# Kernel tuning notes

Hardware: AMD Instinct MI355X
Metric: run time of the kernel (lower is better)

Reference implementation:

```python
import jax, jax.numpy as jnp
import numpy as np
import math

DIM = 768
HEADS = 12
HEAD_DIM = DIM // HEADS
LENS_T = 64
LENS_S = 256
NTOK = LENS_T + LENS_S
BATCH = 32
MLP_HIDDEN = 4 * DIM
KEEP_RATIO = 0.7
LENS_KEEP = math.ceil(KEEP_RATIO * LENS_S)  # 180, static
NEG_INF = -1e9  # finite stand-in for masked_fill(-inf); mask is all-False here
LN_EPS = 1e-5


def layer_norm(x, g, b):
    m = jnp.mean(x, axis=-1, keepdims=True)
    v = jnp.var(x, axis=-1, keepdims=True)
    return (x - m) * jax.lax.rsqrt(v + LN_EPS) * g + b


def attention(x_normed, w_qkv, w_proj, b_proj, mask):
    # x_normed: [B,N,C]; torch: qkv Linear (no bias), split heads, softmax(qk*scale), proj
    B, N, C = x_normed.shape
    qkv = (x_normed @ w_qkv.T).reshape(B, N, 3, HEADS, HEAD_DIM)
    qkv = jnp.transpose(qkv, (2, 0, 3, 1, 4))  # [3,B,H,N,Dh]
    q, k, v = qkv[0], qkv[1], qkv[2]
    scores = jnp.einsum('bhqd,bhkd->bhqk', q, k) * (HEAD_DIM ** -0.5)
    scores = jnp.where(mask[:, None, None, :], NEG_INF, scores)
    attn = jax.nn.softmax(scores, axis=-1)  # [B,H,N,N]
    out = jnp.einsum('bhqk,bhkd->bhqd', attn, v)
    out = jnp.transpose(out, (0, 2, 1, 3)).reshape(B, N, C)
    return out @ w_proj.T + b_proj, attn


def mlp(x, w_fc1, b_fc1, w_fc2, b_fc2):
    h = jax.nn.gelu(x @ w_fc1.T + b_fc1, approximate=False)
    return h @ w_fc2.T + b_fc2


def candidate_topk(attn_all, tmpl_mask_f):
    # attn_all: [B,H,N,N]; template->search block, masked mean over template rows,
    # mean over heads, sort descending, split into keep/removed.
    attn_ts = attn_all[:, :, :LENS_T, LENS_T:]  # [B,H,T,S]
    w = tmpl_mask_f[:, None, :, None]  # [B,1,T,1]
    denom = jnp.sum(tmpl_mask_f, axis=1)[:, None, None]  # [B,1,1]
    scores = jnp.sum(attn_ts * w, axis=2) / denom  # [B,H,S] mean over kept template rows
    scores = jnp.mean(scores, axis=1)  # [B,S] mean over heads
    order = jnp.argsort(-scores, axis=1)  # descending
    return order[:, :LENS_KEEP], order[:, LENS_KEEP:]


def gather_tokens(tokens, topk_idx):
    tokens_t = tokens[:, :LENS_T]
    tokens_s = tokens[:, LENS_T:]
    kept = jnp.take_along_axis(tokens_s, topk_idx[:, :, None], axis=1)
    return jnp.concatenate([tokens_t, kept], axis=1)


def setup_inputs() -> dict:
    key = jax.random.key(0)
    ks = jax.random.split(key, 12)
    s = 0.02
    return {
        'x_rgb': jax.random.normal(ks[0], (BATCH, NTOK, DIM), jnp.float32),
        'x_tir': jax.random.normal(ks[1], (BATCH, NTOK, DIM), jnp.float32),
        'global_index_t': jax.random.randint(ks[2], (BATCH, LENS_T), 0, 64).astype(jnp.int64),
        'global_index_s': jax.random.randint(ks[3], (BATCH, LENS_S), 0, 256).astype(jnp.int64),
        'mask': jnp.zeros((BATCH, NTOK), dtype=bool),
        'cte_template_mask': jnp.ones((BATCH, LENS_T), dtype=bool),
        'keep_ratio_search': 0,
        'js_loss': jax.random.normal(ks[4], (1,), jnp.float32),
        'g1': jnp.ones((DIM,), jnp.float32),
        'b1': jnp.zeros((DIM,), jnp.float32),
        'w_qkv': jax.random.normal(ks[5], (3 * DIM, DIM), jnp.float32) * s,
        'w_proj': jax.random.normal(ks[6], (DIM, DIM), jnp.float32) * s,
        'b_proj': jnp.zeros((DIM,), jnp.float32),
        'g2': jnp.ones((DIM,), jnp.float32),
        'b2': jnp.zeros((DIM,), jnp.float32),
        'w_fc1': jax.random.normal(ks[7], (MLP_HIDDEN, DIM), jnp.float32) * s,
        'b_fc1': jnp.zeros((MLP_HIDDEN,), jnp.float32),
        'w_fc2': jax.random.normal(ks[8], (DIM, MLP_HIDDEN), jnp.float32) * s,
        'b_fc2': jnp.zeros((DIM,), jnp.float32),
    }


def reference(x_rgb, x_tir, global_index_t, global_index_s, mask, cte_template_mask,
              keep_ratio_search, js_loss, g1, b1, w_qkv, w_proj, b_proj, g2, b2,
              w_fc1, b_fc1, w_fc2, b_fc2):
    # dual-stream shared-weight attention
    rgb_attn_out, corrmap_rgb = attention(layer_norm(x_rgb, g1, b1), w_qkv, w_proj, b_proj, mask)
    tir_attn_out, corrmap_tir = attention(layer_norm(x_tir, g1, b1), w_qkv, w_proj, b_proj, mask)
    x_rgb = x_rgb + rgb_attn_out  # drop_path = Identity
    x_tir = x_tir + tir_attn_out

    # candidate elimination: both streams use the SAME fused attention map,
    # so the topk is identical for rgb and tir (torch calls it twice, same result)
    attn_all = corrmap_rgb + corrmap_tir
    tmpl_mask_f = cte_template_mask.astype(attn_all.dtype)
    topk_idx, non_topk_idx = candidate_topk(attn_all, tmpl_mask_f)
    x_rgb = gather_tokens(x_rgb, topk_idx)
    x_tir = gather_tokens(x_tir, topk_idx)
    global_index_s_new = jnp.take_along_axis(global_index_s, topk_idx, axis=1)
    removed_index_s = jnp.take_along_axis(global_index_s, non_topk_idx, axis=1)

    x_rgb = x_rgb + mlp(layer_norm(x_rgb, g2, b2), w_fc1, b_fc1, w_fc2, b_fc2)
    x_tir = x_tir + mlp(layer_norm(x_tir, g2, b2), w_fc1, b_fc1, w_fc2, b_fc2)
    return (x_rgb, x_tir, global_index_t, global_index_s_new, removed_index_s,
            corrmap_rgb, corrmap_tir, js_loss)
```

## Files before the change

### kernel.cpp

```cpp
#include <hip/hip_runtime.h>

typedef long long LL;
typedef unsigned short ushort_t;
typedef __attribute__((ext_vector_type(8))) short bfrag;
typedef __attribute__((ext_vector_type(8))) _Float16 hfrag;
typedef __attribute__((ext_vector_type(4))) float facc;
typedef __attribute__((ext_vector_type(4))) unsigned short us4;

constexpr int CDIM  = 768;
constexpr int HEADS = 12;
constexpr int LT    = 64;
constexpr int NTOK  = 320;
constexpr int BATCH = 32;
constexpr int LKEEP = 180;
constexpr int LREM  = 76;
constexpr int NK    = 244;

constexpr LL O_XRGB = 0;
constexpr LL O_XTIR = 5996544;
constexpr LL O_GIT  = 11993088;
constexpr LL O_GSN  = 11995136;
constexpr LL O_REM  = 12000896;
constexpr LL O_CR   = 12003328;
constexpr LL O_CT   = 51324928;
constexpr LL O_JS   = 90646528;

constexpr LL W_X1   = 0;
constexpr LL W_X1G  = 15728640;
constexpr LL W_XN   = 27746304;
constexpr LL W_QKV  = 35610624;
constexpr LL W_ATT  = 59596800;

constexpr LL SZH = 7864320;

__device__ inline ushort_t cvt_bf16(float f) {
    union { float f; unsigned u; } x; x.f = f;
    unsigned u = x.u + 0x7fffu + ((x.u >> 16) & 1u);
    return (ushort_t)(u >> 16);
}
union h16u { _Float16 h; ushort_t u; };

#define GLL(gp, lp) __builtin_amdgcn_global_load_lds( \
    (const __attribute__((address_space(1))) unsigned int*)(gp), \
    (__attribute__((address_space(3))) unsigned int*)(lp), 16, 0, 0)

template<bool B16OUT>
__global__ __launch_bounds__(256)
void ln_kernel(const float* __restrict__ x, const float* __restrict__ g,
               const float* __restrict__ bta, void* __restrict__ y)
{
    LL row = blockIdx.x;
    const float* xr = x + row * 768;
    int t = threadIdx.x;
    float v0 = xr[t], v1 = xr[t + 256], v2 = xr[t + 512];
    __shared__ float red[256];
    red[t] = v0 + v1 + v2;
    __syncthreads();
    for (int s = 128; s; s >>= 1) { if (t < s) red[t] += red[t + s]; __syncthreads(); }
    float mean = red[0] / 768.0f;
    __syncthreads();
    float d0 = v0 - mean, d1 = v1 - mean, d2 = v2 - mean;
    red[t] = d0 * d0 + d1 * d1 + d2 * d2;
    __syncthreads();
    for (int s = 128; s; s >>= 1) { if (t < s) red[t] += red[t + s]; __syncthreads(); }
    float var = red[0] / 768.0f;
    float rs = 1.0f / sqrtf(var + 1e-5f);
    float o0 = d0 * rs * g[t]       + bta[t];
    float o1 = d1 * rs * g[t + 256] + bta[t + 256];
    float o2 = d2 * rs * g[t + 512] + bta[t + 512];
    if (B16OUT) {
        ushort_t* yr = (ushort_t*)y + row * 768;
        yr[t] = cvt_bf16(o0); yr[t + 256] = cvt_bf16(o1); yr[t + 512] = cvt_bf16(o2);
    } else {
        float* yr = (float*)y + row * 768;
        yr[t] = o0; yr[t + 256] = o1; yr[t + 512] = o2;
    }
}

__global__ __launch_bounds__(256)
void ln_f16x2(const float* __restrict__ x, const float* __restrict__ g,
              const float* __restrict__ bta,
              ushort_t* __restrict__ yh, ushort_t* __restrict__ yl)
{
    LL row = blockIdx.x;
    const float* xr = x + row * 768;
    int t = threadIdx.x;
    float v0 = xr[t], v1 = xr[t + 256], v2 = xr[t + 512];
    __shared__ float red[256];
    red[t] = v0 + v1 + v2;
    __syncthreads();
    for (int s = 128; s; s >>= 1) { if (t < s) red[t] += red[t + s]; __syncthreads(); }
    float mean = red[0] / 768.0f;
    __syncthreads();
    float d0 = v0 - mean, d1 = v1 - mean, d2 = v2 - mean;
    red[t] = d0 * d0 + d1 * d1 + d2 * d2;
    __syncthreads();
    for (int s = 128; s; s >>= 1) { if (t < s) red[t] += red[t + s]; __syncthreads(); }
    float var = red[0] / 768.0f;
    float rs = 1.0f / sqrtf(var + 1e-5f);
    #pragma unroll
    for (int c = 0; c < 3; ++c) {
        float d = (c == 0 ? d0 : c == 1 ? d1 : d2);
        int idx = t + c * 256;
        float o = d * rs * g[idx] + bta[idx];
        h16u hi, lo;
        hi.h = (_Float16)o;
        lo.h = (_Float16)(o - (float)hi.h);
        yh[row * 768 + idx] = hi.u;
        yl[row * 768 + idx] = lo.u;
    }
}

__global__ __launch_bounds__(256)
void cvt_f16x2(const float* __restrict__ in, ushort_t* __restrict__ oh,
               ushort_t* __restrict__ ol, int n)
{
    int i = (blockIdx.x * 256 + threadIdx.x) * 4;
    if (i >= n) return;
    float4 v = *(const float4*)(in + i);
    us4 h, l;
    #pragma unroll
    for (int j = 0; j < 4; ++j) {
        float f = (j == 0 ? v.x : j == 1 ? v.y : j == 2 ? v.z : v.w);
        h16u hh, ll;
        hh.h = (_Float16)f;
        ll.h = (_Float16)(f - (float)hh.h);
        h[j] = hh.u; l[j] = ll.u;
    }
    *(us4*)(oh + i) = h;
    *(us4*)(ol + i) = l;
}

__global__ __launch_bounds__(256)
void gemm_qkv(const ushort_t* __restrict__ Ah, const ushort_t* __restrict__ Al,
              const ushort_t* __restrict__ Bh, const ushort_t* __restrict__ Bl,
              ushort_t* __restrict__ Q1, ushort_t* __restrict__ Q2,
              ushort_t* __restrict__ K1, ushort_t* __restrict__ K2,
              ushort_t* __restrict__ Vt)
{
    __shared__ ushort_t Ahs[8192], Als[8192], Bhs[8192], Bls[8192];
    const int t = threadIdx.x;
    const int wave = t >> 6, lane = t & 63;
    const int wr = wave >> 1, wc = wave & 1;
    const int lr = lane & 15, lh = lane >> 4;
    const LL bm = (LL)blockIdx.y * 128, bn = (LL)blockIdx.x * 128;
    const bool vt = (blockIdx.x >= 12);

    facc acc[4][4];
    #pragma unroll
    for (int i = 0; i < 4; ++i)
        #pragma unroll
        for (int j = 0; j < 4; ++j) acc[i][j] = (facc)(0.0f);

    const LL soff = (bm + wave * 16 + (lane >> 2)) * (LL)768 + (lane & 3) * 8;
    const LL boff = (bn + wave * 16 + (lane >> 2)) * (LL)768 + (lane & 3) * 8;
    const LL a64 = (LL)64 * 768;

    GLL(Ah + soff,       &Ahs[wave * 512]);
    GLL(Ah + soff + a64, &Ahs[2048 + wave * 512]);
    GLL(Bh + boff,       &Bhs[wave * 512]);
    GLL(Bh + boff + a64, &Bhs[2048 + wave * 512]);
    if (!vt) {
        GLL(Al + soff,       &Als[wave * 512]);
        GLL(Al + soff + a64, &Als[2048 + wave * 512]);
        GLL(Bl + boff,       &Bls[wave * 512]);
        GLL(Bl + boff + a64, &Bls[2048 + wave * 512]);
    }
    __syncthreads();

    int cur = 0;
    for (int k0 = 0; k0 < 768; k0 += 32) {
        int nb = (cur ^ 1) * 4096;
        if (k0 + 32 < 768) {
            GLL(Ah + soff + k0 + 32,       &Ahs[nb + wave * 512]);
            GLL(Ah + soff + k0 + 32 + a64, &Ahs[nb + 2048 + wave * 512]);
            GLL(Bh + boff + k0 + 32,       &Bhs[nb + wave * 512]);
            GLL(Bh + boff + k0 + 32 + a64, &Bhs[nb + 2048 + wave * 512]);
            if (!vt) {
                GLL(Al + soff + k0 + 32,       &Als[nb + wave * 512]);
                GLL(Al + soff + k0 + 32 + a64, &Als[nb + 2048 + wave * 512]);
                GLL(Bl + boff + k0 + 32,       &Bls[nb + wave * 512]);
                GLL(Bl + boff + k0 + 32 + a64, &Bls[nb + 2048 + wave * 512]);
            }
        }
        int cb = cur * 4096;
        hfrag ah[4], bh[4];
        #pragma unroll
        for (int mi = 0; mi < 4; ++mi)
            ah[mi] = *(const hfrag*)&Ahs[cb + (wr * 64 + mi * 16 + lr) * 32 + lh * 8];
        #pragma unroll
        for (int ni = 0; ni < 4; ++ni)
            bh[ni] = *(const hfrag*)&Bhs[cb + (wc * 64 + ni * 16 + lr) * 32 + lh * 8];
        if (!vt) {
            hfrag al[4], bl[4];
            #pragma unroll
            for (int mi = 0; mi < 4; ++mi)
                al[mi] = *(const hfrag*)&Als[cb + (wr * 64 + mi * 16 + lr) * 32 + lh * 8];
            #pragma unroll
            for (int ni = 0; ni < 4; ++ni)
                bl[ni] = *(const hfrag*)&Bls[cb + (wc * 64 + ni * 16 + lr) * 32 + lh * 8];
            #pragma unroll
            for (int mi = 0; mi < 4; ++mi)
                #pragma unroll
                for (int ni = 0; ni < 4; ++ni) {
                    acc[mi][ni] = __builtin_amdgcn_mfma_f32_16x16x32_f16(al[mi], bh[ni], acc[mi][ni], 0, 0, 0);
                    acc[mi][ni] = __builtin_amdgcn_mfma_f32_16x16x32_f16(ah[mi], bl[ni], acc[mi][ni], 0, 0, 0);
                    acc[mi][ni] = __builtin_amdgcn_mfma_f32_16x16x32_f16(ah[mi], bh[ni], acc[mi][ni], 0, 0, 0);
                }
        } else {
            #pragma unroll
            for (int mi = 0; mi < 4; ++mi)
                #pragma unroll
                for (int ni = 0; ni < 4; ++ni)
                    acc[mi][ni] = __builtin_amdgcn_mfma_f32_16x16x32_f16(ah[mi], bh[ni], acc[mi][ni], 0, 0, 0);
        }
        __syncthreads();
        cur ^= 1;
    }

    #pragma unroll
    for (int mi = 0; mi < 4; ++mi)
        #pragma unroll
        for (int ni = 0; ni < 4; ++ni)
            #pragma unroll
            for (int j = 0; j < 4; ++j) {
                int r = (int)bm + wr * 64 + mi * 16 + lh * 4 + j;
                int c = (int)bn + wc * 64 + ni * 16 + lr;
                int b = r / 320, tt = r - b * 320;
                int s = c / 768, rem = c - s * 768;
                int h = rem >> 6, d = rem & 63;
                LL hb = (LL)(b * 12 + h) * 20480;
                float v = acc[mi][ni][j];
                if (s == 2) {
                    Vt[hb + d * 320 + tt] = cvt_bf16(v);
                } else {
                    h16u a1, a2;
                    a1.h = (_Float16)v;
                    a2.h = (_Float16)(v - (float)a1.h);
                    LL idx = hb + (LL)tt * 64 + d;
                    if (s == 0) { Q1[idx] = a1.u; Q2[idx] = a2.u; }
                    else        { K1[idx] = a1.u; K2[idx] = a2.u; }
                }
            }
}

__global__ __launch_bounds__(256, 2)
void fused_attn(const ushort_t* __restrict__ Qh, const ushort_t* __restrict__ Qm,
                const ushort_t* __restrict__ Kh, const ushort_t* __restrict__ Km,
                const ushort_t* __restrict__ Vt,
                float* __restrict__ corr, ushort_t* __restrict__ attb,
                double* __restrict__ part, int mod)
{
    __shared__ __align__(128) unsigned char lds[81920];
    constexpr int PS = 40960;

    const int t = threadIdx.x;
    const int wave = t >> 6, lane = t & 63;
    const int lr = lane & 15, lh = lane >> 4;
    const int id  = blockIdx.x;
    const int xcd = id & 7;
    const int rem = id >> 3;
    const int grp = rem / 5;
    const int r0i = rem - grp * 5;
    const int bh  = grp * 8 + xcd;
    const int b = bh / 12, h = bh - b * 12;
    const int r0 = r0i * 64;
    const LL kvbase = (LL)bh * 20480;

    const LL qoff = kvbase + (LL)(r0 + wave * 16 + lr) * 64 + lh * 8;
    hfrag qh0 = *(const hfrag*)(Qh + qoff), qh1 = *(const hfrag*)(Qh + qoff + 32);
    hfrag qm0 = *(const hfrag*)(Qm + qoff), qm1 = *(const hfrag*)(Qm + qoff + 32);

    facc sacc[20];
    #pragma unroll
    for (int ct = 0; ct < 20; ++ct) sacc[ct] = (facc)(0.0f);

    #pragma unroll
    for (int ha = 0; ha < 5; ++ha) {
        if (ha) __syncthreads();
        #pragma unroll
        for (int i = 0; i < 4; ++i) {
            int id2 = wave * 4 + i;
            int s = id2 >> 3, c = id2 & 7;
            int local = c * 1024 + lane * 16;
            int row = local >> 7;
            int sb = local ^ ((row & 7) << 4);
            LL src = kvbase + (LL)ha * 4096 + (sb >> 1);
            const ushort_t* kp = (s == 0) ? Kh : Km;
            GLL(kp + src, &lds[s * 8192 + c * 1024]);
        }
        __syncthreads();

        #pragma unroll
        for (int ctl = 0; ctl < 4; ++ctl) {
            int tokl = ctl * 16 + lr;
            int x = (tokl & 7) << 4;
            const unsigned char* kb = lds + tokl * 128;
            int o0 = (lh * 16) ^ x;
            int o1 = (64 + lh * 16) ^ x;
            hfrag kh0 = *(const hfrag*)(kb + o0);
            hfrag kh1 = *(const hfrag*)(kb + o1);
            hfrag km0 = *(const hfrag*)(kb + 8192 + o0);
            hfrag km1 = *(const hfrag*)(kb + 8192 + o1);
            facc a = sacc[ha * 4 + ctl];
            a = __builtin_amdgcn_mfma_f32_16x16x32_f16(qm0, kh0, a, 0, 0, 0);
            a = __builtin_amdgcn_mfma_f32_16x16x32_f16(qh0, km0, a, 0, 0, 0);
            a = __builtin_amdgcn_mfma_f32_16x16x32_f16(qh0, kh0, a, 0, 0, 0);
            a = __builtin_amdgcn_mfma_f32_16x16x32_f16(qm1, kh1, a, 0, 0, 0);
            a = __builtin_amdgcn_mfma_f32_16x16x32_f16(qh1, km1, a, 0, 0, 0);
            a = __builtin_amdgcn_mfma_f32_16x16x32_f16(qh1, kh1, a, 0, 0, 0);
            sacc[ha * 4 + ctl] = a;
        }
    }

    __syncthreads();

    #pragma unroll
    for (int i = 0; i < 10; ++i) {
        int chunk = wave * 10 + i;
        int gs = chunk * 1024 + lane * 16;
        int d = gs / 640;
        int w = gs - d * 640;
        int sb = d * 640 + (w ^ ((d & 7) << 4));
        GLL(Vt + kvbase + (sb >> 1), &lds[chunk * 1024]);
    }

    float rs4[4];
    #pragma unroll
    for (int j = 0; j < 4; ++j) {
        float m = sacc[0][j];
        #pragma unroll
        for (int ct = 1; ct < 20; ++ct) m = fmaxf(m, sacc[ct][j]);
        #pragma unroll
        for (int o = 1; o < 16; o <<= 1) m = fmaxf(m, __shfl_xor(m, o, 64));
        m *= 0.125f;
        float s = 0.0f;
        #pragma unroll
        for (int ct = 0; ct < 20; ++ct) {
            float e = expf(sacc[ct][j] * 0.125f - m);
            sacc[ct][j] = e;
            s += e;
        }
        #pragma unroll
        for (int o = 1; o < 16; o <<= 1) s += __shfl_xor(s, o, 64);
        float rs = 1.0f / s;
        rs4[j] = rs;

        int prow = wave * 16 + lh * 4 + j;
        int xr = (prow & 7) << 4;
        #pragma unroll
        for (int ct = 0; ct < 20; ++ct) {
            int pcol = ct * 16 + lr;
            *(ushort_t*)(lds + PS + prow * 640 + ((pcol * 2) ^ xr)) =
                cvt_bf16(sacc[ct][j] * rs);
        }
    }

    __syncthreads();

    facc oacc[4];
    #pragma unroll
    for (int dt = 0; dt < 4; ++dt) oacc[dt] = (facc)(0.0f);
    int prow2 = wave * 16 + lr;
    int xp = (prow2 & 7) << 4;
    #pragma unroll
    for (int k0 = 0; k0 < 10; ++k0) {
        bfrag pa = *(const bfrag*)(lds + PS + prow2 * 640 + ((k0 * 64 + lh * 16) ^ xp));
        #pragma unroll
        for (int dt = 0; dt < 4; ++dt) {
            int dcol = dt * 16 + lr;
            bfrag vb = *(const bfrag*)(lds + dcol * 640 + ((k0 * 64 + lh * 16) ^ ((dcol & 7) << 4)));
            oacc[dt] = __builtin_amdgcn_mfma_f32_16x16x32_bf16(pa, vb, oacc[dt], 0, 0, 0);
        }
    }
    #pragma unroll
    for (int dt = 0; dt < 4; ++dt)
        #pragma unroll
        for (int j = 0; j < 4; ++j) {
            int grow = r0 + wave * 16 + lh * 4 + j;
            int gcol = h * 64 + dt * 16 + lr;
            attb[(LL)(b * 320 + grow) * 768 + gcol] = cvt_bf16(oacc[dt][j]);
        }

    __syncthreads();

    #pragma unroll
    for (int ct = 0; ct < 20; ++ct) {
        int pcol = ct * 16 + lr;
        #pragma unroll
        for (int j = 0; j < 4; ++j) {
            int prow = wave * 16 + lh * 4 + j;
            *(float*)(lds + (prow * 320 + pcol) * 4) = sacc[ct][j] * rs4[j];
        }
    }
    __syncthreads();

    float* crow = corr + (LL)bh * 102400 + (LL)r0 * 320;
    #pragma unroll
    for (int i = 0; i < 20; ++i) {
        int idx = i * 256 + t;
        int row = idx / 80, c4 = idx - row * 80;
        float4 v = *(const float4*)(lds + (row * 320 + c4 * 4) * 4);
        *(float4*)(crow + row * 320 + c4 * 4) = v;
    }

    if (r0i == 0) {
        double s64 = 0.0;
        for (int r = 0; r < 64; ++r)
            s64 += (double)*(const float*)(lds + (r * 320 + 64 + t) * 4);
        part[((LL)mod * 384 + bh) * 256 + t] = s64;
    }
}

template<int EPI>
__global__ __launch_bounds__(256)
void gemm_mfma(const ushort_t* __restrict__ A, const ushort_t* __restrict__ B,
               void* __restrict__ Cv, const float* __restrict__ bias,
               const float* __restrict__ res, const int* __restrict__ amap,
               int K, int lda, int ldb, int ldc, int ldres)
{
    __shared__ ushort_t As[8192];
    __shared__ ushort_t Bs[8192];
    const int t = threadIdx.x;
    const int wave = t >> 6, lane = t & 63;
    const int wr = wave >> 1, wc = wave & 1;
    const LL bm = (LL)blockIdx.y * 128, bn = (LL)blockIdx.x * 128;

    facc acc[4][4];
    #pragma unroll
    for (int i = 0; i < 4; ++i)
        #pragma unroll
        for (int j = 0; j < 4; ++j) acc[i][j] = (facc)(0.0f);

    const int lr = lane & 15, lh = lane >> 4;
    int r1 = (int)bm + wave * 16 + (lane >> 2);
    int r2 = r1 + 64;
    if (amap) { r1 = amap[r1]; r2 = amap[r2]; }
    const ushort_t* gA1 = A + (LL)r1 * lda + (lane & 3) * 8;
    const ushort_t* gA2 = A + (LL)r2 * lda + (lane & 3) * 8;
    const ushort_t* gB = B + (bn + wave * 16 + (lane >> 2)) * ldb + (lane & 3) * 8;
    const LL b64 = (LL)64 * ldb;

    GLL(gA1,       &As[wave * 512]);
    GLL(gA2,       &As[2048 + wave * 512]);
    GLL(gB,        &Bs[wave * 512]);
    GLL(gB + b64,  &Bs[2048 + wave * 512]);
    __syncthreads();

    int cur = 0;
    for (int k0 = 0; k0 < K; k0 += 32) {
        int nb = (cur ^ 1) * 4096;
        if (k0 + 32 < K) {
            GLL(gA1 + k0 + 32,       &As[nb + wave * 512]);
            GLL(gA2 + k0 + 32,       &As[nb + 2048 + wave * 512]);
            GLL(gB + k0 + 32,        &Bs[nb + wave * 512]);
            GLL(gB + k0 + 32 + b64,  &Bs[nb + 2048 + wave * 512]);
        }
        int cb = cur * 4096;
        bfrag a[4], b[4];
        #pragma unroll
        for (int m = 0; m < 4; ++m)
            a[m] = *(const bfrag*)&As[cb + (wr * 64 + m * 16 + lr) * 32 + lh * 8];
        #pragma unroll
        for (int n = 0; n < 4; ++n)
            b[n] = *(const bfrag*)&Bs[cb + (wc * 64 + n * 16 + lr) * 32 + lh * 8];
        #pragma unroll
        for (int m = 0; m < 4; ++m)
            #pragma unroll
            for (int n = 0; n < 4; ++n)
                acc[m][n] = __builtin_amdgcn_mfma_f32_16x16x32_bf16(a[m], b[n], acc[m][n], 0, 0, 0);
        __syncthreads();
        cur ^= 1;
    }

    #pragma unroll
    for (int m = 0; m < 4; ++m) {
        #pragma unroll
        for (int n = 0; n < 4; ++n) {
            #pragma unroll
            for (int j = 0; j < 4; ++j) {
                LL r = bm + wr * 64 + m * 16 + lh * 4 + j;
                LL c = bn + wc * 64 + n * 16 + lr;
                float v = acc[m][n][j] + bias[c];
                if (EPI == 1) {
                    v = 0.5f * v * (erff(v * 0.70710678118654752f) + 1.0f);
                    ((ushort_t*)Cv)[r * ldc + c] = cvt_bf16(v);
                } else {
                    LL rr = amap ? (LL)amap[r] : r;
                    v += res[rr * ldres + c];
                    ((float*)Cv)[r * ldc + c] = v;
                }
            }
        }
    }
}

__global__ __launch_bounds__(256)
void f32_to_bf16(const float* __restrict__ in, ushort_t* __restrict__ out, int n)
{
    int i = (blockIdx.x * 256 + threadIdx.x) * 4;
    if (i >= n) return;
    float4 v = *(const float4*)(in + i);
    us4 o;
    o[0] = cvt_bf16(v.x); o[1] = cvt_bf16(v.y);
    o[2] = cvt_bf16(v.z); o[3] = cvt_bf16(v.w);
    *(us4*)(out + i) = o;
}

__global__ __launch_bounds__(256)
void rank_all(const double* __restrict__ part, const int* __restrict__ gis,
              const int* __restrict__ git, const float* __restrict__ js,
              int* __restrict__ srcmap, float* __restrict__ out)
{
    int b = blockIdx.x, j = threadIdx.x;
    double acc = 0.0;
    for (int h = 0; h < 12; ++h) {
        LL i0 = ((LL)(b * 12 + h)) * 256 + j;
        acc += (part[i0] + part[98304 + i0]) / 64.0;
    }
    double sj = acc / 12.0;
    __shared__ double s[256];
    __shared__ int sord[256];
    s[j] = sj;
    __syncthreads();
    int r = 0;
    for (int i = 0; i < 256; ++i) {
        double si = s[i];
        r += (si > sj) || (si == sj && i < j);
    }
    sord[r] = j;
    float gv = (float)gis[b * 256 + j];
    if (r < LKEEP) out[O_GSN + b * LKEEP + r] = gv;
    else           out[O_REM + b * LREM + (r - LKEEP)] = gv;
    __syncthreads();
    if (j < NK) {
        int src = (j < LT) ? j : (LT + sord[j - LT]);
        srcmap[b * NK + j] = b * NTOK + src;
    }
    if (j < 64) out[O_GIT + b * 64 + j] = (float)git[b * 64 + j];
    if (b == 0 && j == 0) out[O_JS] = js[0];
}

extern "C" void kernel_launch(void* const* d_in, const int* in_sizes, int n_in,
                              void* d_out, int out_size, void* d_ws, size_t ws_size,
                              hipStream_t stream)
{
    const float* xin_m[2] = { (const float*)d_in[0], (const float*)d_in[1] };
    const int*   git    = (const int*)d_in[2];
    const int*   gis    = (const int*)d_in[3];
    const float* js     = (const float*)d_in[7];
    const float* g1     = (const float*)d_in[8];
    const float* b1     = (const float*)d_in[9];
    const float* w_qkv  = (const float*)d_in[10];
    const float* w_proj = (const float*)d_in[11];
    const float* b_proj = (const float*)d_in[12];
    const float* g2     = (const float*)d_in[13];
    const float* b2     = (const float*)d_in[14];
    const float* w_fc1  = (const float*)d_in[15];
    const float* b_fc1  = (const float*)d_in[16];
    const float* w_fc2  = (const float*)d_in[17];
    const float* b_fc2  = (const float*)d_in[18];

    float* out = (float*)d_out;
    float* ws  = (float*)d_ws;

    ushort_t* Xh   = (ushort_t*)(ws + W_X1);
    ushort_t* Xl   = Xh + SZH;
    float*    X1c  = ws + W_X1;
    ushort_t* ATTb0 = (ushort_t*)(ws + W_XN);
    ushort_t* ATTb1 = ATTb0 + SZH;
    ushort_t* QK  = (ushort_t*)(ws + W_QKV);
    ushort_t* Qh2 = QK,           *Qm2 = QK + SZH;
    ushort_t* Kh2 = QK + 2 * SZH, *Km2 = QK + 3 * SZH;
    ushort_t* Wh  = (ushort_t*)(ws + W_ATT);
    ushort_t* Wl  = Wh + 1769472;
    ushort_t* Vt  = (ushort_t*)(ws + W_ATT + 2000000);
    double*   part = (double*)(ws + W_ATT + 6000000);
    int*      srcmap = (int*)(ws + W_ATT + 6400000);
    ushort_t* WPROJb = (ushort_t*)(ws + W_X1G);
    ushort_t* WFC1b  = (ushort_t*)(ws + W_ATT);
    ushort_t* WFC2b  = (ushort_t*)(ws + W_ATT + 1179648);
    ushort_t* XN2b   = (ushort_t*)(ws + W_XN);
    ushort_t* H1b    = (ushort_t*)(ws + W_QKV);

    f32_to_bf16<<<dim3(576), dim3(256), 0, stream>>>(w_proj, WPROJb, 589824);
    cvt_f16x2<<<dim3(1728), dim3(256), 0, stream>>>(w_qkv, Wh, Wl, 1769472);

    for (int m = 0; m < 2; ++m) {
        const float* xin = xin_m[m];
        float* corr = out + (m ? O_CT : O_CR);
        ushort_t* ATTbm = m ? ATTb1 : ATTb0;

        ln_f16x2<<<dim3(BATCH * NTOK), dim3(256), 0, stream>>>(xin, g1, b1, Xh, Xl);

        gemm_qkv<<<dim3(18, 80), dim3(256), 0, stream>>>(
            Xh, Xl, Wh, Wl, Qh2, Qm2, Kh2, Km2, Vt);

        fused_attn<<<dim3(1920), dim3(256), 0, stream>>>(
            Qh2, Qm2, Kh2, Km2, Vt, corr, ATTbm, part, m);
    }

    f32_to_bf16<<<dim3(2304), dim3(256), 0, stream>>>(w_fc1, WFC1b, 2359296);
    f32_to_bf16<<<dim3(2304), dim3(256), 0, stream>>>(w_fc2, WFC2b, 2359296);

    rank_all<<<dim3(BATCH), dim3(256), 0, stream>>>(part, gis, git, js, srcmap, out);

    for (int m = 0; m < 2; ++m) {
        gemm_mfma<2><<<dim3(6, 61), dim3(256), 0, stream>>>(
            m ? ATTb1 : ATTb0, WPROJb, X1c + (LL)m * 5996544, b_proj,
            xin_m[m], srcmap, 768, 768, 768, 768, 768);
    }

    ln_kernel<true><<<dim3(2 * BATCH * NK), dim3(256), 0, stream>>>(
        X1c, g2, b2, XN2b);

    gemm_mfma<1><<<dim3(24, 122), dim3(256), 0, stream>>>(
        XN2b, WFC1b, H1b, b_fc1, nullptr, nullptr, 768, 768, 768, 3072, 0);

    gemm_mfma<2><<<dim3(6, 122), dim3(256), 0, stream>>>(
        H1b, WFC2b, out + O_XRGB, b_fc2, X1c, nullptr, 3072, 3072, 3072, 768, 768);
}
```

Before: 962.8 us.

## Merge weight conversions, batch both LayerNorms, add XCD-aware block remapping

The four separate weight conversion kernels become one prep_weights launch. The two per-modality LayerNorm launches are merged into a single launch that writes both streams' split f16 outputs, which moves the fc weight buffers to a different workspace region. Both GEMM kernels gain an XCD-aware block index remap so that neighbouring tiles land on the same chiplet and share L2. The aim is fewer launches and better cache locality, at the cost of more workspace in use at once and a possible overlap of the moved buffers with live data.

```diff
diff --git a/kernel.cpp b/kernel.cpp
--- a/kernel.cpp
+++ b/kernel.cpp
@@ -43,6 +43,63 @@
 #define GLL(gp, lp) __builtin_amdgcn_global_load_lds( \
     (const __attribute__((address_space(1))) unsigned int*)(gp), \
     (__attribute__((address_space(3))) unsigned int*)(lp), 16, 0, 0)
+
+__device__ inline void xcd_decode(int& bx, int& by) {
+    int gx = gridDim.x;
+    int nwg = gx * gridDim.y;
+    int bid = blockIdx.y * gx + blockIdx.x;
+    int q = nwg >> 3, r = nwg & 7;
+    int xcd = bid & 7, i = bid >> 3;
+    int wg = (xcd < r ? xcd * (q + 1) : r * (q + 1) + (xcd - r) * q) + i;
+    bx = wg % gx;
+    by = wg / gx;
+}
+
+__global__ __launch_bounds__(256)
+void prep_weights(const float* __restrict__ wproj, const float* __restrict__ wqkv,
+                  const float* __restrict__ wfc1, const float* __restrict__ wfc2,
+                  ushort_t* __restrict__ WPROJb, ushort_t* __restrict__ Wh,
+                  ushort_t* __restrict__ Wl, ushort_t* __restrict__ WFC1b,
+                  ushort_t* __restrict__ WFC2b)
+{
+    int i = blockIdx.x * 256 + threadIdx.x;
+    if (i < 147456) {
+        int j = i * 4;
+        float4 v = *(const float4*)(wproj + j);
+        us4 o;
+        o[0] = cvt_bf16(v.x); o[1] = cvt_bf16(v.y);
+        o[2] = cvt_bf16(v.z); o[3] = cvt_bf16(v.w);
+        *(us4*)(WPROJb + j) = o;
+    } else if (i < 589824) {
+        int j = (i - 147456) * 4;
+        float4 v = *(const float4*)(wqkv + j);
+        us4 h, l;
+        #pragma unroll
+        for (int k = 0; k < 4; ++k) {
+            float f = (k == 0 ? v.x : k == 1 ? v.y : k == 2 ? v.z : v.w);
+            h16u hh, ll;
+            hh.h = (_Float16)f;
+            ll.h = (_Float16)(f - (float)hh.h);
+            h[k] = hh.u; l[k] = ll.u;
+        }
+        *(us4*)(Wh + j) = h;
+        *(us4*)(Wl + j) = l;
+    } else if (i < 1179648) {
+        int j = (i - 589824) * 4;
+        float4 v = *(const float4*)(wfc1 + j);
+        us4 o;
+        o[0] = cvt_bf16(v.x); o[1] = cvt_bf16(v.y);
+        o[2] = cvt_bf16(v.z); o[3] = cvt_bf16(v.w);
+        *(us4*)(WFC1b + j) = o;
+    } else {
+        int j = (i - 1179648) * 4;
+        float4 v = *(const float4*)(wfc2 + j);
+        us4 o;
+        o[0] = cvt_bf16(v.x); o[1] = cvt_bf16(v.y);
+        o[2] = cvt_bf16(v.z); o[3] = cvt_bf16(v.w);
+        *(us4*)(WFC2b + j) = o;
+    }
+}
 
 template<bool B16OUT>
 __global__ __launch_bounds__(256)
@@ -78,12 +135,16 @@
 }
 
 __global__ __launch_bounds__(256)
-void ln_f16x2(const float* __restrict__ x, const float* __restrict__ g,
-              const float* __restrict__ bta,
-              ushort_t* __restrict__ yh, ushort_t* __restrict__ yl)
-{
-    LL row = blockIdx.x;
-    const float* xr = x + row * 768;
+void ln_f16x2(const float* __restrict__ x0, const float* __restrict__ x1,
+              const float* __restrict__ g, const float* __restrict__ bta,
+              ushort_t* __restrict__ ybase)
+{
+    int row = blockIdx.x;
+    int mod = row >= 10240;
+    int lrow = row - mod * 10240;
+    const float* xr = (mod ? x1 : x0) + (LL)lrow * 768;
+    ushort_t* yh = ybase + (LL)mod * 2 * SZH + (LL)lrow * 768;
+    ushort_t* yl = yh + SZH;
     int t = threadIdx.x;
     float v0 = xr[t], v1 = xr[t + 256], v2 = xr[t + 512];
     __shared__ float red[256];
@@ -106,29 +167,9 @@
         h16u hi, lo;
         hi.h = (_Float16)o;
         lo.h = (_Float16)(o - (float)hi.h);
-        yh[row * 768 + idx] = hi.u;
-        yl[row * 768 + idx] = lo.u;
-    }
-}
-
-__global__ __launch_bounds__(256)
-void cvt_f16x2(const float* __restrict__ in, ushort_t* __restrict__ oh,
-               ushort_t* __restrict__ ol, int n)
-{
-    int i = (blockIdx.x * 256 + threadIdx.x) * 4;
-    if (i >= n) return;
-    float4 v = *(const float4*)(in + i);
-    us4 h, l;
-    #pragma unroll
-    for (int j = 0; j < 4; ++j) {
-        float f = (j == 0 ? v.x : j == 1 ? v.y : j == 2 ? v.z : v.w);
-        h16u hh, ll;
-        hh.h = (_Float16)f;
-        ll.h = (_Float16)(f - (float)hh.h);
-        h[j] = hh.u; l[j] = ll.u;
-    }
-    *(us4*)(oh + i) = h;
-    *(us4*)(ol + i) = l;
+        yh[idx] = hi.u;
+        yl[idx] = lo.u;
+    }
 }
 
 __global__ __launch_bounds__(256)
@@ -139,12 +180,14 @@
               ushort_t* __restrict__ Vt)
 {
     __shared__ ushort_t Ahs[8192], Als[8192], Bhs[8192], Bls[8192];
+    int bx, by;
+    xcd_decode(bx, by);
     const int t = threadIdx.x;
     const int wave = t >> 6, lane = t & 63;
     const int wr = wave >> 1, wc = wave & 1;
     const int lr = lane & 15, lh = lane >> 4;
-    const LL bm = (LL)blockIdx.y * 128, bn = (LL)blockIdx.x * 128;
-    const bool vt = (blockIdx.x >= 12);
+    const LL bm = (LL)by * 128, bn = (LL)bx * 128;
+    const bool vt = (bx >= 12);
 
     facc acc[4][4];
     #pragma unroll
@@ -421,10 +464,12 @@
 {
     __shared__ ushort_t As[8192];
     __shared__ ushort_t Bs[8192];
+    int bx, by;
+    xcd_decode(bx, by);
     const int t = threadIdx.x;
     const int wave = t >> 6, lane = t & 63;
     const int wr = wave >> 1, wc = wave & 1;
-    const LL bm = (LL)blockIdx.y * 128, bn = (LL)blockIdx.x * 128;
+    const LL bm = (LL)by * 128, bn = (LL)bx * 128;
 
     facc acc[4][4];
     #pragma unroll
@@ -496,18 +541,6 @@
 }
 
 __global__ __launch_bounds__(256)
-void f32_to_bf16(const float* __restrict__ in, ushort_t* __restrict__ out, int n)
-{
-    int i = (blockIdx.x * 256 + threadIdx.x) * 4;
-    if (i >= n) return;
-    float4 v = *(const float4*)(in + i);
-    us4 o;
-    o[0] = cvt_bf16(v.x); o[1] = cvt_bf16(v.y);
-    o[2] = cvt_bf16(v.z); o[3] = cvt_bf16(v.w);
-    *(us4*)(out + i) = o;
-}
-
-__global__ __launch_bounds__(256)
 void rank_all(const double* __restrict__ part, const int* __restrict__ gis,
               const int* __restrict__ git, const float* __restrict__ js,
               int* __restrict__ srcmap, float* __restrict__ out)
@@ -564,8 +597,7 @@
     float* out = (float*)d_out;
     float* ws  = (float*)d_ws;
 
-    ushort_t* Xh   = (ushort_t*)(ws + W_X1);
-    ushort_t* Xl   = Xh + SZH;
+    ushort_t* Xbase = (ushort_t*)(ws + W_X1);
     float*    X1c  = ws + W_X1;
     ushort_t* ATTb0 = (ushort_t*)(ws + W_XN);
     ushort_t* ATTb1 = ATTb0 + SZH;
@@ -578,20 +610,22 @@
     double*   part = (double*)(ws + W_ATT + 6000000);
     int*      srcmap = (int*)(ws + W_ATT + 6400000);
     ushort_t* WPROJb = (ushort_t*)(ws + W_X1G);
-    ushort_t* WFC1b  = (ushort_t*)(ws + W_ATT);
-    ushort_t* WFC2b  = (ushort_t*)(ws + W_ATT + 1179648);
+    ushort_t* WFC1b  = (ushort_t*)(ws + W_X1G + 294912);
+    ushort_t* WFC2b  = (ushort_t*)(ws + W_X1G + 1474560);
     ushort_t* XN2b   = (ushort_t*)(ws + W_XN);
     ushort_t* H1b    = (ushort_t*)(ws + W_QKV);
 
-    f32_to_bf16<<<dim3(576), dim3(256), 0, stream>>>(w_proj, WPROJb, 589824);
-    cvt_f16x2<<<dim3(1728), dim3(256), 0, stream>>>(w_qkv, Wh, Wl, 1769472);
+    prep_weights<<<dim3(6912), dim3(256), 0, stream>>>(
+        w_proj, w_qkv, w_fc1, w_fc2, WPROJb, Wh, Wl, WFC1b, WFC2b);
+
+    ln_f16x2<<<dim3(2 * BATCH * NTOK), dim3(256), 0, stream>>>(
+        xin_m[0], xin_m[1], g1, b1, Xbase);
 
     for (int m = 0; m < 2; ++m) {
-        const float* xin = xin_m[m];
         float* corr = out + (m ? O_CT : O_CR);
         ushort_t* ATTbm = m ? ATTb1 : ATTb0;
-
-        ln_f16x2<<<dim3(BATCH * NTOK), dim3(256), 0, stream>>>(xin, g1, b1, Xh, Xl);
+        ushort_t* Xh = Xbase + (LL)m * 2 * SZH;
+        ushort_t* Xl = Xh + SZH;
 
         gemm_qkv<<<dim3(18, 80), dim3(256), 0, stream>>>(
             Xh, Xl, Wh, Wl, Qh2, Qm2, Kh2, Km2, Vt);
@@ -599,9 +633,6 @@
         fused_attn<<<dim3(1920), dim3(256), 0, stream>>>(
             Qh2, Qm2, Kh2, Km2, Vt, corr, ATTbm, part, m);
     }
-
-    f32_to_bf16<<<dim3(2304), dim3(256), 0, stream>>>(w_fc1, WFC1b, 2359296);
-    f32_to_bf16<<<dim3(2304), dim3(256), 0, stream>>>(w_fc2, WFC2b, 2359296);
 
     rank_all<<<dim3(BATCH), dim3(256), 0, stream>>>(part, gis, git, js, srcmap, out);
 
```

Result: faster. 932.8 us (-3.1%).
